# Performance work log

Measured on AMD Instinct MI355X. Metric: run time of the kernel, lower is better.

The kernel has to match this reference:

```python
import jax, jax.numpy as jnp
import numpy as np
from jax import lax

B, T, I, H, N = 8192, 100, 24, 64, 8  # batch, seq_len, input_size, hidden_size, hidden_neurons
H2 = 2 * H


def setup_inputs() -> dict:
    key = jax.random.key(0)
    ks = iter(jax.random.split(key, 80))
    d = {"input_seq": jax.random.normal(next(ks), (B, T, I), jnp.float32)}
    def triple(name, shape):
        d[name + "_mu"] = 0.1 * jax.random.normal(next(ks), shape, jnp.float32)
        d[name + "_rho"] = -6.0 + 0.1 * jax.random.normal(next(ks), shape, jnp.float32)
        d[name + "_eps"] = jax.random.normal(next(ks), shape, jnp.float32)
    # BayesianLSTM params: weight_ih (in, 4H), weight_hh (H, 4H), bias (4H,)
    triple("l1_wih", (I, 4 * H)); triple("l1_whh", (H, 4 * H)); triple("l1_b", (4 * H,))
    triple("l2_wih", (H, 4 * H2)); triple("l2_whh", (H2, 4 * H2)); triple("l2_b", (4 * H2,))
    # BayesianLinear params: weight (out, in), bias (out,)
    triple("fc1_w", (N, H2)); triple("fc1_b", (N,))
    triple("fc2_w", (N, N)); triple("fc2_b", (N,))
    triple("out_w", (1, N)); triple("out_b", (1,))
    return d


def _sample(mu, rho, eps):
    # blitz reparameterization: sigma = log1p(exp(rho))
    return mu + jnp.log1p(jnp.exp(rho)) * eps


def _lstm(x, wih, whh, b):
    # x: [B, T, in]; returns full hidden sequence [B, T, Hn]; gate order i,f,g,o
    Hn = whh.shape[0]
    xg = jnp.einsum('bti,ig->btg', x, wih) + b  # precompute input projection
    def step(carry, xg_t):
        h, c = carry
        gates = xg_t + h @ whh
        i, f, g, o = jnp.split(gates, 4, axis=-1)
        c = jax.nn.sigmoid(f) * c + jax.nn.sigmoid(i) * jnp.tanh(g)
        h = jax.nn.sigmoid(o) * jnp.tanh(c)
        return (h, c), h
    h0 = jnp.zeros((x.shape[0], Hn), x.dtype)
    _, hs = lax.scan(step, (h0, h0), jnp.swapaxes(xg, 0, 1))
    return jnp.swapaxes(hs, 0, 1)


def _forward(input_seq,
             l1_wih_mu, l1_wih_rho, l1_wih_eps, l1_whh_mu, l1_whh_rho, l1_whh_eps,
             l1_b_mu, l1_b_rho, l1_b_eps,
             l2_wih_mu, l2_wih_rho, l2_wih_eps, l2_whh_mu, l2_whh_rho, l2_whh_eps,
             l2_b_mu, l2_b_rho, l2_b_eps,
             fc1_w_mu, fc1_w_rho, fc1_w_eps, fc1_b_mu, fc1_b_rho, fc1_b_eps,
             fc2_w_mu, fc2_w_rho, fc2_w_eps, fc2_b_mu, fc2_b_rho, fc2_b_eps,
             out_w_mu, out_w_rho, out_w_eps, out_b_mu, out_b_rho, out_b_eps):
    w1i = _sample(l1_wih_mu, l1_wih_rho, l1_wih_eps)
    w1h = _sample(l1_whh_mu, l1_whh_rho, l1_whh_eps)
    b1 = _sample(l1_b_mu, l1_b_rho, l1_b_eps)
    w2i = _sample(l2_wih_mu, l2_wih_rho, l2_wih_eps)
    w2h = _sample(l2_whh_mu, l2_whh_rho, l2_whh_eps)
    b2 = _sample(l2_b_mu, l2_b_rho, l2_b_eps)
    fc1w = _sample(fc1_w_mu, fc1_w_rho, fc1_w_eps); fc1b = _sample(fc1_b_mu, fc1_b_rho, fc1_b_eps)
    fc2w = _sample(fc2_w_mu, fc2_w_rho, fc2_w_eps); fc2b = _sample(fc2_b_mu, fc2_b_rho, fc2_b_eps)
    outw = _sample(out_w_mu, out_w_rho, out_w_eps); outb = _sample(out_b_mu, out_b_rho, out_b_eps)

    h1 = _lstm(input_seq, w1i, w1h, b1)      # [B, T, H]
    h2 = _lstm(h1, w2i, w2h, b2)             # [B, T, 2H]
    out = h2[:, -1, :]                       # [B, 2H]
    x = jax.nn.relu(out @ fc1w.T + fc1b)
    x = jax.nn.relu(x @ fc2w.T + fc2b)
    y = x @ outw.T + outb                    # [B, 1]
    return y.reshape(-1)


def reference(input_seq,
              l1_wih_mu, l1_wih_rho, l1_wih_eps, l1_whh_mu, l1_whh_rho, l1_whh_eps,
              l1_b_mu, l1_b_rho, l1_b_eps,
              l2_wih_mu, l2_wih_rho, l2_wih_eps, l2_whh_mu, l2_whh_rho, l2_whh_eps,
              l2_b_mu, l2_b_rho, l2_b_eps,
              fc1_w_mu, fc1_w_rho, fc1_w_eps, fc1_b_mu, fc1_b_rho, fc1_b_eps,
              fc2_w_mu, fc2_w_rho, fc2_w_eps, fc2_b_mu, fc2_b_rho, fc2_b_eps,
              out_w_mu, out_w_rho, out_w_eps, out_b_mu, out_b_rho, out_b_eps):
    return _forward(input_seq,
                    l1_wih_mu, l1_wih_rho, l1_wih_eps, l1_whh_mu, l1_whh_rho, l1_whh_eps,
                    l1_b_mu, l1_b_rho, l1_b_eps,
                    l2_wih_mu, l2_wih_rho, l2_wih_eps, l2_whh_mu, l2_whh_rho, l2_whh_eps,
                    l2_b_mu, l2_b_rho, l2_b_eps,
                    fc1_w_mu, fc1_w_rho, fc1_w_eps, fc1_b_mu, fc1_b_rho, fc1_b_eps,
                    fc2_w_mu, fc2_w_rho, fc2_w_eps, fc2_b_mu, fc2_b_rho, fc2_b_eps,
                    out_w_mu, out_w_rho, out_w_eps, out_b_mu, out_b_rho, out_b_eps)
```

## Files before the change

### kernel.cpp

```cpp
#include <hip/hip_runtime.h>
#include <math.h>


typedef __attribute__((ext_vector_type(8))) short short8;
typedef __attribute__((ext_vector_type(4))) float f32x4;

#define MFMA16(a, b, c) __builtin_amdgcn_mfma_f32_16x16x32_bf16((a), (b), (c), 0, 0, 0)

#define WS_W1G_OFF 196608
#define WS_WF_OFF  245760

struct SampParams {
  const float* w1i[3]; const float* w1h[3]; const float* b1[3];
  const float* w2i[3]; const float* w2h[3]; const float* b2[3];
  const float* f1w[3]; const float* f1b[3];
  const float* f2w[3]; const float* f2b[3];
  const float* ow[3];  const float* ob[3];
  short* W2S; short* W1G; float* WF;
};

struct LstmParams {
  const float* input;
  const short* W2S; const short* W1G; const float* WF;
  float* out;
};

__device__ __forceinline__ float samp(const float* const q[3], int idx) {
  return q[0][idx] + log1pf(expf(q[1][idx])) * q[2][idx];
}

__device__ __forceinline__ short f2bf(float f) {
  unsigned u = __float_as_uint(f);
  unsigned r = (u + 0x7FFFu + ((u >> 16) & 1u)) >> 16;
  return (short)r;
}

__device__ __forceinline__ float sigf(float x) {
  return __builtin_amdgcn_rcpf(1.0f + __builtin_amdgcn_exp2f(-1.44269504f * x));
}
__device__ __forceinline__ float tanhf_(float x) {
  return 1.0f - 2.0f * __builtin_amdgcn_rcpf(1.0f + __builtin_amdgcn_exp2f(2.88539008f * x));
}

__global__ __launch_bounds__(256) void sample_kernel(SampParams p)
{
  int i = blockIdx.x * 256 + threadIdx.x;
  if (i < 12288) {
    int tid = i & 511, gg = (i >> 9) & 3, kk = i >> 11;
    int quad = (tid >> 4) & 3, col = tid & 15, v0 = (tid >> 6) * 16;
    int c = gg * 128 + v0 + col;
    short8 v;
#pragma unroll
    for (int j = 0; j < 8; ++j) {
      int k = kk * 32 + quad * 8 + j;
      float x = (k < 64) ? samp(p.w2i, k * 512 + c) : samp(p.w2h, (k - 64) * 512 + c);
      v[j] = f2bf(x);
    }
    *(short8*)&p.W2S[i * 8] = v;
  } else if (i < 15360) {
    int u = i - 12288;
    int slice = u >> 8, n = u & 255;
    int k0 = (slice >> 2) * 32 + (slice & 3) * 8;
    short8 v;
#pragma unroll
    for (int j = 0; j < 8; ++j) {
      int k = k0 + j;
      float x = 0.0f;
      if (k < 24)       x = samp(p.w1i, k * 256 + n);
      else if (k >= 32) x = samp(p.w1h, (k - 32) * 256 + n);
      v[j] = f2bf(x);
    }
    *(short8*)&p.W1G[u * 8] = v;
  } else if (i < 17241) {
    int u = i - 15360;
    float x;
    if (u < 256)       x = samp(p.b1,  u);
    else if (u < 768)  x = samp(p.b2,  u - 256);
    else if (u < 1792) x = samp(p.f1w, u - 768);
    else if (u < 1856) x = samp(p.f2w, u - 1792);
    else if (u < 1864) x = samp(p.f1b, u - 1856);
    else if (u < 1872) x = samp(p.f2b, u - 1864);
    else if (u < 1880) x = samp(p.ow,  u - 1872);
    else               x = samp(p.ob,  0);
    p.WF[u] = x;
  }
}


__global__ __launch_bounds__(512, 2)
void blstm_kernel(LstmParams p)
{
  __shared__ __align__(16) unsigned char pool[64512];
  short* const W1L = (short*)pool;
  short* const A1  = (short*)(pool + 49152);
  short* const A2  = (short*)(pool + 55808);

  const int tid  = threadIdx.x;
  const int w    = tid >> 6;
  const int l    = tid & 63;
  const int quad = l >> 4;
  const int col  = l & 15;
  const int b0   = blockIdx.x * 32;

  const int wq = w & 3;
  const int mh = w >> 2;
  const int v0 = w * 16;

#pragma unroll
  for (int r = 0; r < 6; ++r) {
    short8 v = *(const short8*)&p.W1G[(r * 512 + tid) * 8];
    *(short8*)&W1L[(r * 512 + tid) * 8] = v;
  }

  float b1v[4], b2v[4];
#pragma unroll
  for (int g = 0; g < 4; ++g) b1v[g] = p.WF[g * 64 + wq * 16 + col];
#pragma unroll
  for (int g = 0; g < 4; ++g) b2v[g] = p.WF[256 + g * 128 + v0 + col];

  for (int i = tid; i < 3328; i += 512) A1[i] = 0;
  for (int i = tid; i < 4352; i += 512) A2[i] = 0;
  __syncthreads();

  int xr = 0, xi = 0;
  const float* xptr = p.input;
  if (tid < 384) {
    int e = tid * 2; xr = e / 24; xi = e - xr * 24;
    const float* base = p.input + (size_t)(b0 + xr) * 2400 + xi;
    float2 xv = *(const float2*)base;
    unsigned pk = (unsigned)(unsigned short)f2bf(xv.x)
                | ((unsigned)(unsigned short)f2bf(xv.y) << 16);
    *(unsigned*)&A1[xr * 104 + xi] = pk;
    xptr = base + 24;
  }
  __syncthreads();

  f32x4 c1 = {0.f, 0.f, 0.f, 0.f};
  f32x4 c2[2]; c2[0] = c1; c2[1] = c1;
  float hf2[2][4];

  const int a1rd = (mh * 16 + col) * 104;
  const short8* const W2v = (const short8*)p.W2S;

  for (int j = 0; j <= 100; ++j) {
    const bool do_x = (j <= 98) && (tid < 384);
    float2 xv;
    if (do_x) xv = *(const float2*)xptr;

    short8 aA0 = *(const short8*)&A1[a1rd +      quad * 8];
    short8 aA1 = *(const short8*)&A1[a1rd + 32 + quad * 8];
    short8 aA2 = *(const short8*)&A1[a1rd + 64 + quad * 8];
    f32x4 g1[4];
#pragma unroll
    for (int g = 0; g < 4; ++g) {
      f32x4 acc = (f32x4){b1v[g], b1v[g], b1v[g], b1v[g]};
      acc = MFMA16(aA0, *(const short8*)&W1L[(((0 * 4 + quad) << 8) + g * 64 + wq * 16 + col) * 8], acc);
      acc = MFMA16(aA1, *(const short8*)&W1L[(((1 * 4 + quad) << 8) + g * 64 + wq * 16 + col) * 8], acc);
      acc = MFMA16(aA2, *(const short8*)&W1L[(((2 * 4 + quad) << 8) + g * 64 + wq * 16 + col) * 8], acc);
      g1[g] = acc;
    }

    f32x4 g2[2][4];
#pragma unroll
    for (int g = 0; g < 4; ++g) {
      g2[0][g] = (f32x4){b2v[g], b2v[g], b2v[g], b2v[g]};
      g2[1][g] = g2[0][g];
    }
#pragma unroll
    for (int kk = 0; kk < 6; ++kk) {
      short8 w0 = W2v[(kk * 4 + 0) * 512 + tid];
      short8 w1 = W2v[(kk * 4 + 1) * 512 + tid];
      short8 w2 = W2v[(kk * 4 + 2) * 512 + tid];
      short8 w3 = W2v[(kk * 4 + 3) * 512 + tid];
      short8 a0, a1f;
      if (kk < 2) {
        a0  = *(const short8*)&A1[      col  * 104 + 32 + kk * 32 + quad * 8];
        a1f = *(const short8*)&A1[(16 + col) * 104 + 32 + kk * 32 + quad * 8];
      } else {
        int o = (kk - 2) * 32 + quad * 8;
        a0  = *(const short8*)&A2[      col  * 136 + o];
        a1f = *(const short8*)&A2[(16 + col) * 136 + o];
      }
      g2[0][0] = MFMA16(a0,  w0, g2[0][0]);
      g2[0][1] = MFMA16(a0,  w1, g2[0][1]);
      g2[0][2] = MFMA16(a0,  w2, g2[0][2]);
      g2[0][3] = MFMA16(a0,  w3, g2[0][3]);
      g2[1][0] = MFMA16(a1f, w0, g2[1][0]);
      g2[1][1] = MFMA16(a1f, w1, g2[1][1]);
      g2[1][2] = MFMA16(a1f, w2, g2[1][2]);
      g2[1][3] = MFMA16(a1f, w3, g2[1][3]);
    }

    short hb1[4];
#pragma unroll
    for (int i = 0; i < 4; ++i) {
      float iv = sigf(g1[0][i]);
      float fv = sigf(g1[1][i]);
      float gv = tanhf_(g1[2][i]);
      float ov = sigf(g1[3][i]);
      float cn = fv * c1[i] + iv * gv;
      c1[i] = cn;
      hb1[i] = f2bf(ov * tanhf_(cn));
    }

    short hb2[2][4];
    if (j) {
#pragma unroll
      for (int mi = 0; mi < 2; ++mi)
#pragma unroll
        for (int i = 0; i < 4; ++i) {
          float iv = sigf(g2[mi][0][i]);
          float fv = sigf(g2[mi][1][i]);
          float gv = tanhf_(g2[mi][2][i]);
          float ov = sigf(g2[mi][3][i]);
          float cn = fv * c2[mi][i] + iv * gv;
          c2[mi][i] = cn;
          float hv = ov * tanhf_(cn);
          hf2[mi][i] = hv;
          hb2[mi][i] = f2bf(hv);
        }
    }
    __syncthreads();

    {
      int u = wq * 16 + col;
#pragma unroll
      for (int i = 0; i < 4; ++i) {
        int row = mh * 16 + quad * 4 + i;
        A1[row * 104 + 32 + u] = hb1[i];
      }
      if (do_x) {
        unsigned pk = (unsigned)(unsigned short)f2bf(xv.x)
                    | ((unsigned)(unsigned short)f2bf(xv.y) << 16);
        *(unsigned*)&A1[xr * 104 + xi] = pk;
      }
      if (j) {
        int u2 = v0 + col;
#pragma unroll
        for (int mi = 0; mi < 2; ++mi)
#pragma unroll
          for (int i = 0; i < 4; ++i) {
            int row = mi * 16 + quad * 4 + i;
            A2[row * 136 + u2] = hb2[mi][i];
          }
      }
    }
    __syncthreads();
    xptr += 24;
  }

  float* const H2   = (float*)pool;
  float* const FC1W = (float*)(pool + 16896);
  float* const FC2W = (float*)(pool + 20992);
  float* const FB1  = (float*)(pool + 21248);
  float* const FB2  = (float*)(pool + 21280);
  float* const OWp  = (float*)(pool + 21312);
  float* const OBp  = (float*)(pool + 21344);
  float* const X1   = (float*)(pool + 21376);
  float* const X2   = (float*)(pool + 22400);

  {
    int u2 = v0 + col;
#pragma unroll
    for (int mi = 0; mi < 2; ++mi)
#pragma unroll
      for (int i = 0; i < 4; ++i) {
        int row = mi * 16 + quad * 4 + i;
        H2[row * 132 + u2] = hf2[mi][i];
      }
  }
  for (int i = tid; i < 1024; i += 512) FC1W[i] = p.WF[768 + i];
  if (tid < 64)               FC2W[tid]     = p.WF[1792 + tid];
  if (tid >= 64 && tid < 72)  FB1[tid - 64] = p.WF[1856 + tid - 64];
  if (tid >= 72 && tid < 80)  FB2[tid - 72] = p.WF[1864 + tid - 72];
  if (tid >= 80 && tid < 88)  OWp[tid - 80] = p.WF[1872 + tid - 80];
  if (tid == 88)              OBp[0]        = p.WF[1880];
  __syncthreads();

  if (tid < 256) {
    int row = tid >> 3, o = tid & 7;
    float s = FB1[o];
#pragma unroll 8
    for (int k = 0; k < 128; ++k) s += H2[row * 132 + k] * FC1W[o * 128 + k];
    X1[tid] = fmaxf(s, 0.0f);
  }
  __syncthreads();
  if (tid < 256) {
    int row = tid >> 3, o = tid & 7;
    float s = FB2[o];
#pragma unroll
    for (int k = 0; k < 8; ++k) s += X1[row * 8 + k] * FC2W[o * 8 + k];
    X2[tid] = fmaxf(s, 0.0f);
  }
  __syncthreads();
  if (tid < 32) {
    float s = OBp[0];
#pragma unroll
    for (int k = 0; k < 8; ++k) s += X2[tid * 8 + k] * OWp[k];
    p.out[b0 + tid] = s;
  }
}

extern "C" void kernel_launch(void* const* d_in, const int* in_sizes, int n_in,
                              void* d_out, int out_size, void* d_ws, size_t ws_size,
                              hipStream_t stream)
{
  (void)in_sizes; (void)n_in; (void)ws_size; (void)out_size;

  SampParams sp;
  const float** grp[12] = { sp.w1i, sp.w1h, sp.b1, sp.w2i, sp.w2h, sp.b2,
                            sp.f1w, sp.f1b, sp.f2w, sp.f2b, sp.ow, sp.ob };
  int idx = 1;
  for (int t = 0; t < 12; ++t)
    for (int j = 0; j < 3; ++j)
      grp[t][j] = (const float*)d_in[idx++];
  sp.W2S = (short*)d_ws;
  sp.W1G = (short*)((char*)d_ws + WS_W1G_OFF);
  sp.WF  = (float*)((char*)d_ws + WS_WF_OFF);

  LstmParams bp;
  bp.input = (const float*)d_in[0];
  bp.W2S = (const short*)d_ws;
  bp.W1G = (const short*)((char*)d_ws + WS_W1G_OFF);
  bp.WF  = (const float*)((char*)d_ws + WS_WF_OFF);
  bp.out = (float*)d_out;

  sample_kernel<<<dim3(68), dim3(256), 0, stream>>>(sp);
  blstm_kernel<<<dim3(256), dim3(512), 0, stream>>>(bp);
}
```

Baseline: 495.9 us.

## Double-buffer LDS hidden states and keep layer-2 weights in registers

Splits the A1/A2 hidden-state tiles in shared memory into ping-pong buffers. Each step reads the previous step's buffer and writes the other, which removes one __syncthreads per timestep. The layer-1 activation and stores now run right after the layer-1 MFMAs instead of after layer 2. The 24 layer-2 recurrent weight fragments are loaded into registers once before the loop instead of being re-read from global memory every timestep. In exchange, shared memory per block grows to about 78 KB and roughly 96 more VGPRs are needed under launch_bounds(512,2), which risks register spilling or lower occupancy.

```diff
diff --git a/kernel.cpp b/kernel.cpp
--- a/kernel.cpp
+++ b/kernel.cpp
@@ -90,10 +90,10 @@
 __global__ __launch_bounds__(512, 2)
 void blstm_kernel(LstmParams p)
 {
-  __shared__ __align__(16) unsigned char pool[64512];
+  __shared__ __align__(16) unsigned char pool[79872];
   short* const W1L = (short*)pool;
-  short* const A1  = (short*)(pool + 49152);
-  short* const A2  = (short*)(pool + 55808);
+  short* const A1b = (short*)(pool + 49152);
+  short* const A2b = (short*)(pool + 62464);
 
   const int tid  = threadIdx.x;
   const int w    = tid >> 6;
@@ -106,6 +106,11 @@
   const int mh = w >> 2;
   const int v0 = w * 16;
 
+  const short8* const W2v = (const short8*)p.W2S;
+  short8 w2r[24];
+#pragma unroll
+  for (int f = 0; f < 24; ++f) w2r[f] = W2v[f * 512 + tid];
+
 #pragma unroll
   for (int r = 0; r < 6; ++r) {
     short8 v = *(const short8*)&p.W1G[(r * 512 + tid) * 8];
@@ -118,8 +123,8 @@
 #pragma unroll
   for (int g = 0; g < 4; ++g) b2v[g] = p.WF[256 + g * 128 + v0 + col];
 
-  for (int i = tid; i < 3328; i += 512) A1[i] = 0;
-  for (int i = tid; i < 4352; i += 512) A2[i] = 0;
+  for (int i = tid; i < 6656; i += 512) A1b[i] = 0;
+  for (int i = tid; i < 8704; i += 512) A2b[i] = 0;
   __syncthreads();
 
   int xr = 0, xi = 0;
@@ -130,7 +135,7 @@
     float2 xv = *(const float2*)base;
     unsigned pk = (unsigned)(unsigned short)f2bf(xv.x)
                 | ((unsigned)(unsigned short)f2bf(xv.y) << 16);
-    *(unsigned*)&A1[xr * 104 + xi] = pk;
+    *(unsigned*)&A1b[xr * 104 + xi] = pk;
     xptr = base + 24;
   }
   __syncthreads();
@@ -140,16 +145,21 @@
   float hf2[2][4];
 
   const int a1rd = (mh * 16 + col) * 104;
-  const short8* const W2v = (const short8*)p.W2S;
 
   for (int j = 0; j <= 100; ++j) {
+    const int pb = j & 1;
+    const short* const A1r = A1b + pb * 3328;
+    const short* const A2r = A2b + pb * 4352;
+    short* const A1w = A1b + (pb ^ 1) * 3328;
+    short* const A2w = A2b + (pb ^ 1) * 4352;
+
     const bool do_x = (j <= 98) && (tid < 384);
     float2 xv;
     if (do_x) xv = *(const float2*)xptr;
 
-    short8 aA0 = *(const short8*)&A1[a1rd +      quad * 8];
-    short8 aA1 = *(const short8*)&A1[a1rd + 32 + quad * 8];
-    short8 aA2 = *(const short8*)&A1[a1rd + 64 + quad * 8];
+    short8 aA0 = *(const short8*)&A1r[a1rd +      quad * 8];
+    short8 aA1 = *(const short8*)&A1r[a1rd + 32 + quad * 8];
+    short8 aA2 = *(const short8*)&A1r[a1rd + 64 + quad * 8];
     f32x4 g1[4];
 #pragma unroll
     for (int g = 0; g < 4; ++g) {
@@ -160,6 +170,25 @@
       g1[g] = acc;
     }
 
+    {
+      int u = wq * 16 + col;
+#pragma unroll
+      for (int i = 0; i < 4; ++i) {
+        float iv = sigf(g1[0][i]);
+        float fv = sigf(g1[1][i]);
+        float gv = tanhf_(g1[2][i]);
+        float ov = sigf(g1[3][i]);
+        float cn = fv * c1[i] + iv * gv;
+        c1[i] = cn;
+        A1w[(mh * 16 + quad * 4 + i) * 104 + 32 + u] = f2bf(ov * tanhf_(cn));
+      }
+    }
+    if (do_x) {
+      unsigned pk = (unsigned)(unsigned short)f2bf(xv.x)
+                  | ((unsigned)(unsigned short)f2bf(xv.y) << 16);
+      *(unsigned*)&A1w[xr * 104 + xi] = pk;
+    }
+
     f32x4 g2[2][4];
 #pragma unroll
     for (int g = 0; g < 4; ++g) {
@@ -168,43 +197,24 @@
     }
 #pragma unroll
     for (int kk = 0; kk < 6; ++kk) {
-      short8 w0 = W2v[(kk * 4 + 0) * 512 + tid];
-      short8 w1 = W2v[(kk * 4 + 1) * 512 + tid];
-      short8 w2 = W2v[(kk * 4 + 2) * 512 + tid];
-      short8 w3 = W2v[(kk * 4 + 3) * 512 + tid];
       short8 a0, a1f;
       if (kk < 2) {
-        a0  = *(const short8*)&A1[      col  * 104 + 32 + kk * 32 + quad * 8];
-        a1f = *(const short8*)&A1[(16 + col) * 104 + 32 + kk * 32 + quad * 8];
+        a0  = *(const short8*)&A1r[      col  * 104 + 32 + kk * 32 + quad * 8];
+        a1f = *(const short8*)&A1r[(16 + col) * 104 + 32 + kk * 32 + quad * 8];
       } else {
         int o = (kk - 2) * 32 + quad * 8;
-        a0  = *(const short8*)&A2[      col  * 136 + o];
-        a1f = *(const short8*)&A2[(16 + col) * 136 + o];
+        a0  = *(const short8*)&A2r[      col  * 136 + o];
+        a1f = *(const short8*)&A2r[(16 + col) * 136 + o];
       }
-      g2[0][0] = MFMA16(a0,  w0, g2[0][0]);
-      g2[0][1] = MFMA16(a0,  w1, g2[0][1]);
-      g2[0][2] = MFMA16(a0,  w2, g2[0][2]);
-      g2[0][3] = MFMA16(a0,  w3, g2[0][3]);
-      g2[1][0] = MFMA16(a1f, w0, g2[1][0]);
-      g2[1][1] = MFMA16(a1f, w1, g2[1][1]);
-      g2[1][2] = MFMA16(a1f, w2, g2[1][2]);
-      g2[1][3] = MFMA16(a1f, w3, g2[1][3]);
-    }
-
-    short hb1[4];
-#pragma unroll
-    for (int i = 0; i < 4; ++i) {
-      float iv = sigf(g1[0][i]);
-      float fv = sigf(g1[1][i]);
-      float gv = tanhf_(g1[2][i]);
-      float ov = sigf(g1[3][i]);
-      float cn = fv * c1[i] + iv * gv;
-      c1[i] = cn;
-      hb1[i] = f2bf(ov * tanhf_(cn));
-    }
-
-    short hb2[2][4];
+#pragma unroll
+      for (int g = 0; g < 4; ++g) {
+        g2[0][g] = MFMA16(a0,  w2r[kk * 4 + g], g2[0][g]);
+        g2[1][g] = MFMA16(a1f, w2r[kk * 4 + g], g2[1][g]);
+      }
+    }
+
     if (j) {
+      int u2 = v0 + col;
 #pragma unroll
       for (int mi = 0; mi < 2; ++mi)
 #pragma unroll
@@ -217,33 +227,8 @@
           c2[mi][i] = cn;
           float hv = ov * tanhf_(cn);
           hf2[mi][i] = hv;
-          hb2[mi][i] = f2bf(hv);
+          A2w[(mi * 16 + quad * 4 + i) * 136 + u2] = f2bf(hv);
         }
-    }
-    __syncthreads();
-
-    {
-      int u = wq * 16 + col;
-#pragma unroll
-      for (int i = 0; i < 4; ++i) {
-        int row = mh * 16 + quad * 4 + i;
-        A1[row * 104 + 32 + u] = hb1[i];
-      }
-      if (do_x) {
-        unsigned pk = (unsigned)(unsigned short)f2bf(xv.x)
-                    | ((unsigned)(unsigned short)f2bf(xv.y) << 16);
-        *(unsigned*)&A1[xr * 104 + xi] = pk;
-      }
-      if (j) {
-        int u2 = v0 + col;
-#pragma unroll
-        for (int mi = 0; mi < 2; ++mi)
-#pragma unroll
-          for (int i = 0; i < 4; ++i) {
-            int row = mi * 16 + quad * 4 + i;
-            A2[row * 136 + u2] = hb2[mi][i];
-          }
-      }
     }
     __syncthreads();
     xptr += 24;
```

After: 416.2 us. 16.1% less time.
